# Performance work log

Measured on AMD Instinct MI355X. Metric: run time of the kernel, lower is better.

Reference implementation:

```python
import jax, jax.numpy as jnp
import numpy as np

INNER = 4
AFFECT_W = 0.3
LN_EPS = 1e-5


def _ln(x, w, b):
    m = x.mean(-1, keepdims=True)
    v = ((x - m) ** 2).mean(-1, keepdims=True)
    return (x - m) * jax.lax.rsqrt(v + LN_EPS) * w + b


def _gelu(x):
    return jax.nn.gelu(x, approximate=False)  # torch default erf GELU


def setup_inputs() -> dict:
    key = jax.random.key(0)
    ks = jax.random.split(key, 24)
    B, D = 32768, 128
    s = 0.02
    inp = {
        "x": jax.random.normal(ks[0], (B, D), jnp.float32),
        "y_init": jax.random.normal(ks[1], (B, D), jnp.float32),
        "affect_vec": jax.random.normal(ks[2], (B, 3), jnp.float32),
        # LayerNorms
        "ln_lat_w": jnp.ones((3 * D,), jnp.float32), "ln_lat_b": jnp.zeros((3 * D,), jnp.float32),
        "ln_ans_w": jnp.ones((2 * D,), jnp.float32), "ln_ans_b": jnp.zeros((2 * D,), jnp.float32),
        "ln_z_w": jnp.ones((D,), jnp.float32), "ln_z_b": jnp.zeros((D,), jnp.float32),
        # latent MLP: 3D -> 2D -> D
        "W_lat1": jax.random.normal(ks[3], (3 * D, 2 * D), jnp.float32) * s, "b_lat1": jnp.zeros((2 * D,), jnp.float32),
        "W_lat2": jax.random.normal(ks[4], (2 * D, D), jnp.float32) * s, "b_lat2": jnp.zeros((D,), jnp.float32),
        # answer MLP: 2D -> 2D -> D
        "W_ans1": jax.random.normal(ks[5], (2 * D, 2 * D), jnp.float32) * s, "b_ans1": jnp.zeros((2 * D,), jnp.float32),
        "W_ans2": jax.random.normal(ks[6], (2 * D, D), jnp.float32) * s, "b_ans2": jnp.zeros((D,), jnp.float32),
        # affect proj 3 -> D (tanh), gate 2D -> 1 (sigmoid)
        "W_ap": jax.random.normal(ks[7], (3, D), jnp.float32) * s, "b_ap": jnp.zeros((D,), jnp.float32),
        "W_ag": jax.random.normal(ks[8], (2 * D, 1), jnp.float32) * s, "b_ag": jnp.zeros((1,), jnp.float32),
        # tiny single-head self-attention (q,k,v projections)
        "Wq": jax.random.normal(ks[9], (D, D), jnp.float32) * s, "bq": jnp.zeros((D,), jnp.float32),
        "Wk": jax.random.normal(ks[10], (D, D), jnp.float32) * s, "bk": jnp.zeros((D,), jnp.float32),
        "Wv": jax.random.normal(ks[11], (D, D), jnp.float32) * s, "bv": jnp.zeros((D,), jnp.float32),
        "W_p1": jax.random.normal(ks[12], (D, D // 2), jnp.float32) * s, "b_p1": jnp.zeros((D // 2,), jnp.float32),
        "W_p2": jax.random.normal(ks[13], (D // 2, 3), jnp.float32) * s, "b_p2": jnp.zeros((3,), jnp.float32),
        "K": 5,
    }
    return inp


def reference(x, y_init, affect_vec,
              ln_lat_w, ln_lat_b, ln_ans_w, ln_ans_b, ln_z_w, ln_z_b,
              W_lat1, b_lat1, W_lat2, b_lat2,
              W_ans1, b_ans1, W_ans2, b_ans2,
              W_ap, b_ap, W_ag, b_ag,
              Wq, bq, Wk, bk, Wv, bv,
              W_p1, b_p1, W_p2, b_p2, K):
    D = x.shape[-1]
    scale = 1.0 / jnp.sqrt(jnp.asarray(D, x.dtype))
    y = y_init
    z = jnp.zeros_like(y)
    confs = []
    history = []  # list of [B,1,D]
    for k in range(K):
        for n in range(INNER):
            li = _ln(jnp.concatenate([x, y, z], axis=-1), ln_lat_w, ln_lat_b)
            z_delta = _gelu(li @ W_lat1 + b_lat1) @ W_lat2 + b_lat2
            z = _ln(z + 0.3 * z_delta, ln_z_w, ln_z_b)
        affect_latent = jnp.tanh(affect_vec @ W_ap + b_ap)          # [B,D]
        gate = jax.nn.sigmoid(jnp.concatenate([z, affect_latent], axis=-1) @ W_ag + b_ag)  # [B,1]
        z = z + AFFECT_W * gate * affect_latent
        confs.append(gate.mean())
        history.append(z[:, None, :])
        if len(history) > 1:
            seq = jnp.concatenate(history, axis=1)                   # [B,t,D], t<=K
            q = seq @ Wq + bq
            kk = seq @ Wk + bk
            v = seq @ Wv + bv
            att = jax.nn.softmax(jnp.einsum('btd,bsd->bts', q, kk) * scale, axis=-1)
            attn_out = jnp.einsum('bts,bsd->btd', att, v)
            z = _ln(z + attn_out[:, -1, :], ln_z_w, ln_z_b)
        ai = _ln(jnp.concatenate([y, z], axis=-1), ln_ans_w, ln_ans_b)
        y = y + 0.4 * (_gelu(ai @ W_ans1 + b_ans1) @ W_ans2 + b_ans2)
    pad = jnp.tanh(_gelu(z @ W_p1 + b_p1) @ W_p2 + b_p2)             # [B,3]
    return y, jnp.stack(confs), pad
```

## Files before the change

### kernel.cpp

```cpp
#include <hip/hip_runtime.h>
#include <hip/hip_bf16.h>
#include <math.h>


constexpr int NB = 32768;
constexpr int ND = 128;
constexpr float LNEPS = 1e-5f;

typedef short bf16x8 __attribute__((ext_vector_type(8)));
typedef float f32x4 __attribute__((ext_vector_type(4)));
typedef unsigned uint4v __attribute__((ext_vector_type(4)));
using bf16 = __hip_bfloat16;

static __device__ __forceinline__ float gelu_erf(float x) {
  return 0.5f * x * (1.0f + erff(x * 0.70710678118654752440f));
}
static __device__ __forceinline__ float sigmoidf_(float x) {
  return 1.0f / (1.0f + expf(-x));
}
static __device__ __forceinline__ f32x4 mfma16(bf16x8 a, bf16x8 b, f32x4 c) {
  return __builtin_amdgcn_mfma_f32_16x16x32_bf16(a, b, c, 0, 0, 0);
}
static __device__ __forceinline__ float bfs2f(short u) {
  unsigned v = ((unsigned)(unsigned short)u) << 16;
  return __builtin_bit_cast(float, v);
}
static __device__ __forceinline__ unsigned pk_bf2(float a, float b) {
  unsigned ua = __builtin_bit_cast(unsigned, a);
  unsigned ub = __builtin_bit_cast(unsigned, b);
  ua = (ua + 0x7fffu + ((ua >> 16) & 1u)) >> 16;
  ub = (ub + 0x7fffu + ((ub >> 16) & 1u)) & 0xffff0000u;
  return ub | ua;
}

__global__ void prep_w_frag(const float* __restrict__ src, bf16* __restrict__ dst,
                            int K, int N) {
  int i = blockIdx.x * 256 + threadIdx.x;
  if (i >= K * N) return;
  int k = i / N, n = i - k * N;
  int f = ((n >> 4) * (K >> 5) + (k >> 5)) * 512 + (n & 15) * 32 + (k & 31);
  dst[f] = __float2bfloat16(src[i]);
}

__global__ void prep_w1p(const float* __restrict__ W1, const float* __restrict__ lnw,
                         bf16* __restrict__ WXY, bf16* __restrict__ WZ) {
  int i = blockIdx.x * 256 + threadIdx.x;
  if (i >= 384 * 256) return;
  int j = i >> 8, n = i & 255;
  float v = lnw[j] * W1[i];
  if (j < 256) {
    int f = ((n >> 4) * 8 + (j >> 5)) * 512 + (n & 15) * 32 + (j & 31);
    WXY[f] = __float2bfloat16(v);
  } else {
    int k = j - 256;
    int f = ((n >> 4) * 4 + (k >> 5)) * 512 + (n & 15) * 32 + (k & 31);
    WZ[f] = __float2bfloat16(v);
  }
}

__global__ void prep_uv(const float* __restrict__ W1, const float* __restrict__ lnw,
                        const float* __restrict__ lnb, const float* __restrict__ b1,
                        float* __restrict__ U, float* __restrict__ V0b) {
  int n = threadIdx.x;
  float u = 0.f, v = 0.f;
  for (int j = 0; j < 384; ++j) {
    float w = W1[j * 256 + n];
    u = fmaf(lnw[j], w, u);
    v = fmaf(lnb[j], w, v);
  }
  U[n] = u;
  V0b[n] = v + b1[n];
}

__global__ __launch_bounds__(512) void trm_step(
    const float* __restrict__ x, float* __restrict__ y,
    float* __restrict__ z,
    const bf16* __restrict__ W1XYF, const bf16* __restrict__ W1ZF,
    const float* __restrict__ U, const float* __restrict__ V0b,
    const bf16* __restrict__ W2F, const float* __restrict__ b2,
    const float* __restrict__ lzw, const float* __restrict__ lzb,
    const float* __restrict__ av_g,
    const float* __restrict__ lnw_ans, const float* __restrict__ lnb_ans,
    const bf16* __restrict__ WA1F, const float* __restrict__ ba1,
    const bf16* __restrict__ WA2F, const float* __restrict__ ba2,
    const float* __restrict__ Wap, const float* __restrict__ bap,
    const float* __restrict__ Wag, const float* __restrict__ bag,
    const bf16* __restrict__ WqF, const float* __restrict__ bq,
    const bf16* __restrict__ WkF, const float* __restrict__ bk,
    const bf16* __restrict__ WvF, const float* __restrict__ bv,
    float* __restrict__ gate_sum,
    bf16* __restrict__ kh, bf16* __restrict__ vh, int k)
{
  __shared__ __align__(16) char pool[153600];
  __shared__ float gsum[8];
  float (* const zs)[132] = (float(*)[132])pool;
  float (* const ys)[132] = (float(*)[132])(pool + 33792);
  char* const scr = pool + 67584;
  bf16* const pxy  = (bf16*)scr;
  bf16* const znbL = (bf16*)(scr + 33792);
  bf16* const hx   = (bf16*)(scr + 51200);
  bf16* const znbT = (bf16*)scr;
  bf16* const qvb  = (bf16*)(scr + 17408);
  bf16* const kcb  = (bf16*)(scr + 34816);
  bf16* const vcb  = (bf16*)(scr + 52224);
  bf16* const ai   = (bf16*)scr;
  bf16* const ha   = (bf16*)(scr + 33792);
  float2* const sxy = (float2*)(pool + 152576);
  float2* const mr  = (float2*)(pool + 153088);

  const int t = threadIdx.x;
  const int wave = t >> 6, lane = t & 63;
  const int row8 = t >> 3, sub8 = t & 7;
  const int arow = lane & 15, kseg = (lane >> 4) * 8, crow = (lane >> 4) * 4;
  const size_t row0 = (size_t)blockIdx.x * 64;
  const size_t gr = row0 + row8;

  {
    float s = 0.f, ss = 0.f;
    float4 xv[4], yv[4];
    const float4* xp = (const float4*)&x[gr * ND + sub8 * 16];
    const float4* yp = (const float4*)&y[gr * ND + sub8 * 16];
#pragma unroll
    for (int q = 0; q < 4; ++q) { xv[q] = xp[q]; yv[q] = yp[q]; }
#pragma unroll
    for (int q = 0; q < 4; ++q) {
      s += xv[q].x + xv[q].y + xv[q].z + xv[q].w +
           yv[q].x + yv[q].y + yv[q].z + yv[q].w;
      ss += xv[q].x * xv[q].x + xv[q].y * xv[q].y + xv[q].z * xv[q].z + xv[q].w * xv[q].w +
            yv[q].x * yv[q].x + yv[q].y * yv[q].y + yv[q].z * yv[q].z + yv[q].w * yv[q].w;
    }
#pragma unroll
    for (int q = 0; q < 4; ++q) {
      *(unsigned*)&hx[row8 * 264 + sub8 * 16 + q * 4]       = pk_bf2(xv[q].x, xv[q].y);
      *(unsigned*)&hx[row8 * 264 + sub8 * 16 + q * 4 + 2]   = pk_bf2(xv[q].z, xv[q].w);
      *(unsigned*)&hx[row8 * 264 + 128 + sub8 * 16 + q * 4]     = pk_bf2(yv[q].x, yv[q].y);
      *(unsigned*)&hx[row8 * 264 + 128 + sub8 * 16 + q * 4 + 2] = pk_bf2(yv[q].z, yv[q].w);
      *(float4*)&ys[row8][sub8 * 16 + q * 4] = yv[q];
    }
#pragma unroll
    for (int o = 1; o < 8; o <<= 1) { s += __shfl_xor(s, o); ss += __shfl_xor(ss, o); }

    float zsum = 0.f, zss = 0.f;
    float4 zv[4];
    const float4* zp = (const float4*)&z[gr * ND + sub8 * 16];
#pragma unroll
    for (int q = 0; q < 4; ++q) zv[q] = zp[q];
#pragma unroll
    for (int q = 0; q < 4; ++q) {
      *(float4*)&zs[row8][sub8 * 16 + q * 4] = zv[q];
      *(unsigned*)&znbL[row8 * 136 + sub8 * 16 + q * 4]     = pk_bf2(zv[q].x, zv[q].y);
      *(unsigned*)&znbL[row8 * 136 + sub8 * 16 + q * 4 + 2] = pk_bf2(zv[q].z, zv[q].w);
      zsum += zv[q].x + zv[q].y + zv[q].z + zv[q].w;
      zss += zv[q].x * zv[q].x + zv[q].y * zv[q].y + zv[q].z * zv[q].z + zv[q].w * zv[q].w;
    }
#pragma unroll
    for (int o = 1; o < 8; o <<= 1) { zsum += __shfl_xor(zsum, o); zss += __shfl_xor(zss, o); }
    if (sub8 == 0) {
      sxy[row8] = make_float2(s, ss);
      float mm = (s + zsum) * (1.f / 384.f);
      float var = (ss + zss) * (1.f / 384.f) - mm * mm;
      mr[row8] = make_float2(mm, rsqrtf(var + LNEPS));
    }
  }
  __syncthreads();

  {
    f32x4 acc[4][2];
#pragma unroll
    for (int mi = 0; mi < 4; ++mi)
#pragma unroll
      for (int ni = 0; ni < 2; ++ni) acc[mi][ni] = (f32x4){0.f, 0.f, 0.f, 0.f};
#pragma unroll
    for (int kt = 0; kt < 8; ++kt) {
      bf16x8 a[4];
#pragma unroll
      for (int mi = 0; mi < 4; ++mi)
        a[mi] = *(const bf16x8*)&hx[(mi * 16 + arow) * 264 + kt * 32 + kseg];
#pragma unroll
      for (int ni = 0; ni < 2; ++ni) {
        bf16x8 b = *(const bf16x8*)&W1XYF[(size_t)((wave * 2 + ni) * 8 + kt) * 512 +
                                          arow * 32 + kseg];
        acc[0][ni] = mfma16(a[0], b, acc[0][ni]);
        acc[1][ni] = mfma16(a[1], b, acc[1][ni]);
        acc[2][ni] = mfma16(a[2], b, acc[2][ni]);
        acc[3][ni] = mfma16(a[3], b, acc[3][ni]);
      }
    }
#pragma unroll
    for (int ni = 0; ni < 2; ++ni) {
      int col = (wave * 2 + ni) * 16 + arow;
#pragma unroll
      for (int mi = 0; mi < 4; ++mi)
#pragma unroll
        for (int r = 0; r < 4; ++r)
          pxy[(mi * 16 + crow + r) * 264 + col] = __float2bfloat16(acc[mi][ni][r]);
    }
  }
  __syncthreads();

  float Uv[2], Vv[2];
#pragma unroll
  for (int ni = 0; ni < 2; ++ni) {
    int col = (wave * 2 + ni) * 16 + arow;
    Uv[ni] = U[col];
    Vv[ni] = V0b[col];
  }
  const float b2v = b2[wave * 16 + arow];

  for (int n = 0; n < 4; ++n) {
    {
      f32x4 acc[4][2];
#pragma unroll
      for (int mi = 0; mi < 4; ++mi)
#pragma unroll
        for (int ni = 0; ni < 2; ++ni) acc[mi][ni] = (f32x4){0.f, 0.f, 0.f, 0.f};
#pragma unroll
      for (int kt = 0; kt < 4; ++kt) {
        bf16x8 a[4];
#pragma unroll
        for (int mi = 0; mi < 4; ++mi)
          a[mi] = *(const bf16x8*)&znbL[(mi * 16 + arow) * 136 + kt * 32 + kseg];
#pragma unroll
        for (int ni = 0; ni < 2; ++ni) {
          bf16x8 b = *(const bf16x8*)&W1ZF[(size_t)((wave * 2 + ni) * 4 + kt) * 512 +
                                           arow * 32 + kseg];
          acc[0][ni] = mfma16(a[0], b, acc[0][ni]);
          acc[1][ni] = mfma16(a[1], b, acc[1][ni]);
          acc[2][ni] = mfma16(a[2], b, acc[2][ni]);
          acc[3][ni] = mfma16(a[3], b, acc[3][ni]);
        }
      }
#pragma unroll
      for (int ni = 0; ni < 2; ++ni) {
        int col = (wave * 2 + ni) * 16 + arow;
#pragma unroll
        for (int mi = 0; mi < 4; ++mi)
#pragma unroll
          for (int r = 0; r < 4; ++r) {
            int row = mi * 16 + crow + r;
            float2 mrv = mr[row];
            float pv = __bfloat162float(pxy[row * 264 + col]);
            float hpre = mrv.y * (acc[mi][ni][r] + pv - mrv.x * Uv[ni]) + Vv[ni];
            hx[row * 264 + col] = __float2bfloat16(gelu_erf(hpre));
          }
      }
    }
    __syncthreads();

    {
      f32x4 acc2[4];
#pragma unroll
      for (int mi = 0; mi < 4; ++mi) acc2[mi] = (f32x4){0.f, 0.f, 0.f, 0.f};
#pragma unroll
      for (int kt = 0; kt < 8; ++kt) {
        bf16x8 b = *(const bf16x8*)&W2F[(size_t)(wave * 8 + kt) * 512 + arow * 32 + kseg];
#pragma unroll
        for (int mi = 0; mi < 4; ++mi) {
          bf16x8 a = *(const bf16x8*)&hx[(mi * 16 + arow) * 264 + kt * 32 + kseg];
          acc2[mi] = mfma16(a, b, acc2[mi]);
        }
      }
      int col = wave * 16 + arow;
#pragma unroll
      for (int mi = 0; mi < 4; ++mi)
#pragma unroll
        for (int r = 0; r < 4; ++r)
          zs[mi * 16 + crow + r][col] += 0.3f * (acc2[mi][r] + b2v);
    }
    __syncthreads();

    {
      float4 v[4];
#pragma unroll
      for (int q = 0; q < 4; ++q) v[q] = *(const float4*)&zs[row8][sub8 * 16 + q * 4];
      float s = 0.f, ss = 0.f;
#pragma unroll
      for (int q = 0; q < 4; ++q) {
        s += v[q].x + v[q].y + v[q].z + v[q].w;
        ss += v[q].x * v[q].x + v[q].y * v[q].y + v[q].z * v[q].z + v[q].w * v[q].w;
      }
#pragma unroll
      for (int o = 1; o < 8; o <<= 1) { s += __shfl_xor(s, o); ss += __shfl_xor(ss, o); }
      float m = s * (1.f / 128.f);
      float rstd = rsqrtf(ss * (1.f / 128.f) - m * m + LNEPS);
      float os = 0.f, oss = 0.f;
#pragma unroll
      for (int q = 0; q < 4; ++q) {
        float4 w = *(const float4*)&lzw[sub8 * 16 + q * 4];
        float4 b = *(const float4*)&lzb[sub8 * 16 + q * 4];
        float4 o4;
        o4.x = (v[q].x - m) * rstd * w.x + b.x;
        o4.y = (v[q].y - m) * rstd * w.y + b.y;
        o4.z = (v[q].z - m) * rstd * w.z + b.z;
        o4.w = (v[q].w - m) * rstd * w.w + b.w;
        *(float4*)&zs[row8][sub8 * 16 + q * 4] = o4;
        *(unsigned*)&znbL[row8 * 136 + sub8 * 16 + q * 4]     = pk_bf2(o4.x, o4.y);
        *(unsigned*)&znbL[row8 * 136 + sub8 * 16 + q * 4 + 2] = pk_bf2(o4.z, o4.w);
        os += o4.x + o4.y + o4.z + o4.w;
        oss += o4.x * o4.x + o4.y * o4.y + o4.z * o4.z + o4.w * o4.w;
      }
#pragma unroll
      for (int o = 1; o < 8; o <<= 1) { os += __shfl_xor(os, o); oss += __shfl_xor(oss, o); }
      if (sub8 == 0) {
        float2 sv = sxy[row8];
        float mm = (sv.x + os) * (1.f / 384.f);
        float var = (sv.y + oss) * (1.f / 384.f) - mm * mm;
        mr[row8] = make_float2(mm, rsqrtf(var + LNEPS));
      }
    }
    __syncthreads();
  }

  {
    float zf[16];
#pragma unroll
    for (int q = 0; q < 4; ++q) {
      float4 v = *(const float4*)&zs[row8][sub8 * 16 + q * 4];
      zf[q * 4 + 0] = v.x; zf[q * 4 + 1] = v.y;
      zf[q * 4 + 2] = v.z; zf[q * 4 + 3] = v.w;
    }
    float a0 = av_g[gr * 3 + 0], a1 = av_g[gr * 3 + 1], a2 = av_g[gr * 3 + 2];
    float alf[16];
    float s = 0.f;
#pragma unroll
    for (int e = 0; e < 16; ++e) {
      int c = sub8 * 16 + e;
      alf[e] = tanhf(fmaf(a0, Wap[c], fmaf(a1, Wap[128 + c], fmaf(a2, Wap[256 + c], bap[c]))));
      s += zf[e] * Wag[c] + alf[e] * Wag[128 + c];
    }
#pragma unroll
    for (int o = 1; o < 8; o <<= 1) s += __shfl_xor(s, o);
    float g = sigmoidf_(s + bag[0]);
    float gv = (sub8 == 0) ? g : 0.f;
#pragma unroll
    for (int o = 1; o < 64; o <<= 1) gv += __shfl_xor(gv, o);
    if (lane == 0) gsum[wave] = gv;
#pragma unroll
    for (int e = 0; e < 16; ++e) zf[e] = fmaf(0.3f * g, alf[e], zf[e]);
#pragma unroll
    for (int q = 0; q < 4; ++q) {
      float4 o4;
      o4.x = zf[q * 4 + 0]; o4.y = zf[q * 4 + 1];
      o4.z = zf[q * 4 + 2]; o4.w = zf[q * 4 + 3];
      *(float4*)&zs[row8][sub8 * 16 + q * 4] = o4;
      *(unsigned*)&znbT[row8 * 136 + sub8 * 16 + q * 4]     = pk_bf2(o4.x, o4.y);
      *(unsigned*)&znbT[row8 * 136 + sub8 * 16 + q * 4 + 2] = pk_bf2(o4.z, o4.w);
    }
  }
  __syncthreads();
  if (t == 0) {
    float gs = 0.f;
#pragma unroll
    for (int w = 0; w < 8; ++w) gs += gsum[w];
    atomicAdd(gate_sum + k, gs);
  }

  {
    f32x4 aq[4], ak[4], av2[4];
#pragma unroll
    for (int mi = 0; mi < 4; ++mi) {
      aq[mi] = (f32x4){0.f, 0.f, 0.f, 0.f};
      ak[mi] = (f32x4){0.f, 0.f, 0.f, 0.f};
      av2[mi] = (f32x4){0.f, 0.f, 0.f, 0.f};
    }
#pragma unroll
    for (int kt = 0; kt < 4; ++kt) {
      size_t wr = (size_t)(wave * 4 + kt) * 512 + arow * 32 + kseg;
      bf16x8 bqv = *(const bf16x8*)&WqF[wr];
      bf16x8 bkv = *(const bf16x8*)&WkF[wr];
      bf16x8 bvv = *(const bf16x8*)&WvF[wr];
#pragma unroll
      for (int mi = 0; mi < 4; ++mi) {
        bf16x8 a = *(const bf16x8*)&znbT[(mi * 16 + arow) * 136 + kt * 32 + kseg];
        aq[mi] = mfma16(a, bqv, aq[mi]);
        ak[mi] = mfma16(a, bkv, ak[mi]);
        av2[mi] = mfma16(a, bvv, av2[mi]);
      }
    }
    int col = wave * 16 + arow;
    float bqs = bq[col], bks = bk[col], bvs = bv[col];
#pragma unroll
    for (int mi = 0; mi < 4; ++mi)
#pragma unroll
      for (int r = 0; r < 4; ++r) {
        int row = mi * 16 + crow + r;
        qvb[row * 136 + col] = __float2bfloat16(aq[mi][r] + bqs);
        kcb[row * 136 + col] = __float2bfloat16(ak[mi][r] + bks);
        vcb[row * 136 + col] = __float2bfloat16(av2[mi][r] + bvs);
      }
  }
  __syncthreads();

  if (k < 4) {
    uint4v k0 = *(const uint4v*)&kcb[row8 * 136 + sub8 * 16];
    uint4v k1 = *(const uint4v*)&kcb[row8 * 136 + sub8 * 16 + 8];
    uint4v v0 = *(const uint4v*)&vcb[row8 * 136 + sub8 * 16];
    uint4v v1 = *(const uint4v*)&vcb[row8 * 136 + sub8 * 16 + 8];
    size_t off = ((size_t)k * NB + gr) * ND + sub8 * 16;
    __builtin_nontemporal_store(k0, (uint4v*)&kh[off]);
    __builtin_nontemporal_store(k1, (uint4v*)&kh[off + 8]);
    __builtin_nontemporal_store(v0, (uint4v*)&vh[off]);
    __builtin_nontemporal_store(v1, (uint4v*)&vh[off + 8]);
  }
  {
    float zf[16];
#pragma unroll
    for (int q = 0; q < 4; ++q) {
      float4 v = *(const float4*)&zs[row8][sub8 * 16 + q * 4];
      zf[q * 4 + 0] = v.x; zf[q * 4 + 1] = v.y;
      zf[q * 4 + 2] = v.z; zf[q * 4 + 3] = v.w;
    }
    if (k > 0) {
      bf16x8 qv0 = *(const bf16x8*)&qvb[row8 * 136 + sub8 * 16];
      bf16x8 qv1 = *(const bf16x8*)&qvb[row8 * 136 + sub8 * 16 + 8];
      float p[5];
#pragma unroll
      for (int s = 0; s < 5; ++s) {
        if (s > k) break;
        bf16x8 k0, k1;
        if (s == k) {
          k0 = *(const bf16x8*)&kcb[row8 * 136 + sub8 * 16];
          k1 = *(const bf16x8*)&kcb[row8 * 136 + sub8 * 16 + 8];
        } else {
          size_t off = ((size_t)s * NB + gr) * ND + sub8 * 16;
          k0 = __builtin_bit_cast(bf16x8, __builtin_nontemporal_load((const uint4v*)&kh[off]));
          k1 = __builtin_bit_cast(bf16x8, __builtin_nontemporal_load((const uint4v*)&kh[off + 8]));
        }
        float d = 0.f;
#pragma unroll
        for (int e = 0; e < 8; ++e)
          d += bfs2f(qv0[e]) * bfs2f(k0[e]) + bfs2f(qv1[e]) * bfs2f(k1[e]);
#pragma unroll
        for (int o = 1; o < 8; o <<= 1) d += __shfl_xor(d, o);
        p[s] = d * 0.088388347648318447f;
      }
      float mx = p[0];
#pragma unroll
      for (int s = 1; s < 5; ++s) if (s <= k) mx = fmaxf(mx, p[s]);
      float sum = 0.f;
#pragma unroll
      for (int s = 0; s < 5; ++s) if (s <= k) { p[s] = expf(p[s] - mx); sum += p[s]; }
      float inv = 1.f / sum;
      float ao[16];
#pragma unroll
      for (int e = 0; e < 16; ++e) ao[e] = 0.f;
#pragma unroll
      for (int s = 0; s < 5; ++s) {
        if (s > k) break;
        bf16x8 v0, v1;
        if (s == k) {
          v0 = *(const bf16x8*)&vcb[row8 * 136 + sub8 * 16];
          v1 = *(const bf16x8*)&vcb[row8 * 136 + sub8 * 16 + 8];
        } else {
          size_t off = ((size_t)s * NB + gr) * ND + sub8 * 16;
          v0 = __builtin_bit_cast(bf16x8, __builtin_nontemporal_load((const uint4v*)&vh[off]));
          v1 = __builtin_bit_cast(bf16x8, __builtin_nontemporal_load((const uint4v*)&vh[off + 8]));
        }
        float w = p[s] * inv;
#pragma unroll
        for (int e = 0; e < 8; ++e) {
          ao[e]     = fmaf(w, bfs2f(v0[e]), ao[e]);
          ao[8 + e] = fmaf(w, bfs2f(v1[e]), ao[8 + e]);
        }
      }
#pragma unroll
      for (int e = 0; e < 16; ++e) zf[e] += ao[e];
      float s2 = 0.f, ss = 0.f;
#pragma unroll
      for (int e = 0; e < 16; ++e) { s2 += zf[e]; ss += zf[e] * zf[e]; }
#pragma unroll
      for (int o = 1; o < 8; o <<= 1) { s2 += __shfl_xor(s2, o); ss += __shfl_xor(ss, o); }
      float m = s2 * (1.f / 128.f);
      float rstd = rsqrtf(ss * (1.f / 128.f) - m * m + LNEPS);
#pragma unroll
      for (int e = 0; e < 16; ++e) {
        int c = sub8 * 16 + e;
        zf[e] = (zf[e] - m) * rstd * lzw[c] + lzb[c];
      }
#pragma unroll
      for (int q = 0; q < 4; ++q) {
        float4 o4;
        o4.x = zf[q * 4 + 0]; o4.y = zf[q * 4 + 1];
        o4.z = zf[q * 4 + 2]; o4.w = zf[q * 4 + 3];
        *(float4*)&zs[row8][sub8 * 16 + q * 4] = o4;
      }
    }
#pragma unroll
    for (int q = 0; q < 4; ++q) {
      float4 o4;
      o4.x = zf[q * 4 + 0]; o4.y = zf[q * 4 + 1];
      o4.z = zf[q * 4 + 2]; o4.w = zf[q * 4 + 3];
      *(float4*)&z[gr * ND + sub8 * 16 + q * 4] = o4;
    }
  }
  __syncthreads();

  {
    float yf[16], zf[16];
#pragma unroll
    for (int q = 0; q < 4; ++q) {
      float4 v = *(const float4*)&ys[row8][sub8 * 16 + q * 4];
      yf[q * 4 + 0] = v.x; yf[q * 4 + 1] = v.y;
      yf[q * 4 + 2] = v.z; yf[q * 4 + 3] = v.w;
      float4 w = *(const float4*)&zs[row8][sub8 * 16 + q * 4];
      zf[q * 4 + 0] = w.x; zf[q * 4 + 1] = w.y;
      zf[q * 4 + 2] = w.z; zf[q * 4 + 3] = w.w;
    }
    float s = 0.f, ss = 0.f;
#pragma unroll
    for (int e = 0; e < 16; ++e) {
      s += yf[e] + zf[e];
      ss += yf[e] * yf[e] + zf[e] * zf[e];
    }
#pragma unroll
    for (int o = 1; o < 8; o <<= 1) { s += __shfl_xor(s, o); ss += __shfl_xor(ss, o); }
    float m = s * (1.f / 256.f);
    float rstd = rsqrtf(ss * (1.f / 256.f) - m * m + LNEPS);
#pragma unroll
    for (int h = 0; h < 2; ++h) {
      const float* vp = (h == 0) ? yf : zf;
#pragma unroll
      for (int q = 0; q < 4; ++q) {
        int c0 = h * 128 + sub8 * 16 + q * 4;
        float a0 = (vp[q * 4 + 0] - m) * rstd * lnw_ans[c0 + 0] + lnb_ans[c0 + 0];
        float a1 = (vp[q * 4 + 1] - m) * rstd * lnw_ans[c0 + 1] + lnb_ans[c0 + 1];
        float a2 = (vp[q * 4 + 2] - m) * rstd * lnw_ans[c0 + 2] + lnb_ans[c0 + 2];
        float a3 = (vp[q * 4 + 3] - m) * rstd * lnw_ans[c0 + 3] + lnb_ans[c0 + 3];
        *(unsigned*)&ai[row8 * 264 + c0]     = pk_bf2(a0, a1);
        *(unsigned*)&ai[row8 * 264 + c0 + 2] = pk_bf2(a2, a3);
      }
    }
  }
  __syncthreads();

  {
    f32x4 acc[4][2];
#pragma unroll
    for (int mi = 0; mi < 4; ++mi)
#pragma unroll
      for (int ni = 0; ni < 2; ++ni) acc[mi][ni] = (f32x4){0.f, 0.f, 0.f, 0.f};
#pragma unroll
    for (int kt = 0; kt < 8; ++kt) {
      bf16x8 a[4];
#pragma unroll
      for (int mi = 0; mi < 4; ++mi)
        a[mi] = *(const bf16x8*)&ai[(mi * 16 + arow) * 264 + kt * 32 + kseg];
#pragma unroll
      for (int ni = 0; ni < 2; ++ni) {
        bf16x8 b = *(const bf16x8*)&WA1F[(size_t)((wave * 2 + ni) * 8 + kt) * 512 +
                                         arow * 32 + kseg];
        acc[0][ni] = mfma16(a[0], b, acc[0][ni]);
        acc[1][ni] = mfma16(a[1], b, acc[1][ni]);
        acc[2][ni] = mfma16(a[2], b, acc[2][ni]);
        acc[3][ni] = mfma16(a[3], b, acc[3][ni]);
      }
    }
#pragma unroll
    for (int ni = 0; ni < 2; ++ni) {
      int col = (wave * 2 + ni) * 16 + arow;
      float bb = ba1[col];
#pragma unroll
      for (int mi = 0; mi < 4; ++mi)
#pragma unroll
        for (int r = 0; r < 4; ++r)
          ha[(mi * 16 + crow + r) * 264 + col] =
              __float2bfloat16(gelu_erf(acc[mi][ni][r] + bb));
    }
  }
  __syncthreads();

  {
    f32x4 acc[4];
#pragma unroll
    for (int mi = 0; mi < 4; ++mi) acc[mi] = (f32x4){0.f, 0.f, 0.f, 0.f};
#pragma unroll
    for (int kt = 0; kt < 8; ++kt) {
      bf16x8 b = *(const bf16x8*)&WA2F[(size_t)(wave * 8 + kt) * 512 + arow * 32 + kseg];
#pragma unroll
      for (int mi = 0; mi < 4; ++mi) {
        bf16x8 a = *(const bf16x8*)&ha[(mi * 16 + arow) * 264 + kt * 32 + kseg];
        acc[mi] = mfma16(a, b, acc[mi]);
      }
    }
    int col = wave * 16 + arow;
    float bb = ba2[col];
#pragma unroll
    for (int mi = 0; mi < 4; ++mi)
#pragma unroll
      for (int r = 0; r < 4; ++r)
        ys[mi * 16 + crow + r][col] += 0.4f * (acc[mi][r] + bb);
  }
  __syncthreads();

#pragma unroll
  for (int q = 0; q < 4; ++q)
    *(float4*)&y[gr * ND + sub8 * 16 + q * 4] =
        *(const float4*)&ys[row8][sub8 * 16 + q * 4];
}

__global__ __launch_bounds__(256) void pad_head(
    const float* __restrict__ z,
    const float* __restrict__ W1, const float* __restrict__ b1,
    const float* __restrict__ W2, const float* __restrict__ b2,
    float* __restrict__ out)
{
  __shared__ __align__(16) float zsm[32][132];
  __shared__ __align__(16) float h[32][68];
  const int t = threadIdx.x;
  const int row0 = blockIdx.x * 32;
  {
    const int c = t & 127, rg = t >> 7;
#pragma unroll
    for (int r16 = 0; r16 < 16; ++r16) {
      int r = rg * 16 + r16;
      zsm[r][c] = z[(size_t)(row0 + r) * ND + c];
    }
  }
  __syncthreads();
  {
    const int c = t & 63, rg8 = t >> 6;
    float acc[8];
#pragma unroll
    for (int r = 0; r < 8; ++r) acc[r] = 0.f;
    for (int j0 = 0; j0 < ND; j0 += 4) {
      float w0 = W1[(j0 + 0) * 64 + c], w1 = W1[(j0 + 1) * 64 + c];
      float w2 = W1[(j0 + 2) * 64 + c], w3 = W1[(j0 + 3) * 64 + c];
#pragma unroll
      for (int r = 0; r < 8; ++r) {
        float4 a = *reinterpret_cast<const float4*>(&zsm[rg8 * 8 + r][j0]);
        acc[r] = fmaf(a.x, w0, fmaf(a.y, w1, fmaf(a.z, w2, fmaf(a.w, w3, acc[r]))));
      }
    }
    float bb = b1[c];
#pragma unroll
    for (int r = 0; r < 8; ++r) h[rg8 * 8 + r][c] = gelu_erf(acc[r] + bb);
  }
  __syncthreads();
  {
    const int row = t >> 3, sub = t & 7;
    if (sub < 3) {
      float p = 0.f;
      for (int j = 0; j < 64; ++j) p += h[row][j] * W2[j * 3 + sub];
      out[(size_t)(row0 + row) * 3 + sub] = tanhf(p + b2[sub]);
    }
  }
}

__global__ void finalize_confs(const float* __restrict__ gs, float* __restrict__ confs) {
  int i = threadIdx.x;
  if (i < 5) confs[i] = gs[i] * (1.0f / 32768.0f);
}

extern "C" void kernel_launch(void* const* d_in, const int* in_sizes, int n_in,
                              void* d_out, int out_size, void* d_ws, size_t ws_size,
                              hipStream_t stream) {
  const float* x       = (const float*)d_in[0];
  const float* y_init  = (const float*)d_in[1];
  const float* av      = (const float*)d_in[2];
  const float* ln_lat_w = (const float*)d_in[3];
  const float* ln_lat_b = (const float*)d_in[4];
  const float* ln_ans_w = (const float*)d_in[5];
  const float* ln_ans_b = (const float*)d_in[6];
  const float* ln_z_w   = (const float*)d_in[7];
  const float* ln_z_b   = (const float*)d_in[8];
  const float* W_lat1 = (const float*)d_in[9];  const float* b_lat1 = (const float*)d_in[10];
  const float* W_lat2 = (const float*)d_in[11]; const float* b_lat2 = (const float*)d_in[12];
  const float* W_ans1 = (const float*)d_in[13]; const float* b_ans1 = (const float*)d_in[14];
  const float* W_ans2 = (const float*)d_in[15]; const float* b_ans2 = (const float*)d_in[16];
  const float* W_ap = (const float*)d_in[17];   const float* b_ap = (const float*)d_in[18];
  const float* W_ag = (const float*)d_in[19];   const float* b_ag = (const float*)d_in[20];
  const float* Wq = (const float*)d_in[21];     const float* bq = (const float*)d_in[22];
  const float* Wk = (const float*)d_in[23];     const float* bk = (const float*)d_in[24];
  const float* Wv = (const float*)d_in[25];     const float* bv = (const float*)d_in[26];
  const float* W_p1 = (const float*)d_in[27];   const float* b_p1 = (const float*)d_in[28];
  const float* W_p2 = (const float*)d_in[29];   const float* b_p2 = (const float*)d_in[30];

  float* y     = (float*)d_out;
  float* confs = (float*)d_out + (size_t)NB * ND;
  float* pad   = confs + 5;

  char* p = (char*)d_ws;
  float* gate_sum = (float*)p;
  float* z   = (float*)(p + 256);
  bf16* kh   = (bf16*)(p + 256 + (size_t)NB * ND * 4);
  bf16* vh   = kh + (size_t)4 * NB * ND;
  bf16* W2F  = vh + (size_t)4 * NB * ND;
  bf16* WA1F = W2F + 256 * 128;
  bf16* WA2F = WA1F + 256 * 256;
  bf16* WqF  = WA2F + 256 * 128;
  bf16* WkF  = WqF + 128 * 128;
  bf16* WvF  = WkF + 128 * 128;
  bf16* W1XYF = WvF + 128 * 128;
  bf16* W1ZF  = W1XYF + 256 * 256;
  float* U    = (float*)(W1ZF + 128 * 256);
  float* V0b  = U + 256;

  hipMemcpyAsync(y, y_init, (size_t)NB * ND * sizeof(float),
                 hipMemcpyDeviceToDevice, stream);
  hipMemsetAsync(gate_sum, 0, 32, stream);
  hipMemsetAsync(z, 0, (size_t)NB * ND * sizeof(float), stream);

  prep_w1p<<<(384 * 256 + 255) / 256, 256, 0, stream>>>(W_lat1, ln_lat_w, W1XYF, W1ZF);
  prep_uv<<<1, 256, 0, stream>>>(W_lat1, ln_lat_w, ln_lat_b, b_lat1, U, V0b);
  prep_w_frag<<<(256 * 128 + 255) / 256, 256, 0, stream>>>(W_lat2, W2F, 256, 128);
  prep_w_frag<<<(256 * 256 + 255) / 256, 256, 0, stream>>>(W_ans1, WA1F, 256, 256);
  prep_w_frag<<<(256 * 128 + 255) / 256, 256, 0, stream>>>(W_ans2, WA2F, 256, 128);
  prep_w_frag<<<(128 * 128 + 255) / 256, 256, 0, stream>>>(Wq, WqF, 128, 128);
  prep_w_frag<<<(128 * 128 + 255) / 256, 256, 0, stream>>>(Wk, WkF, 128, 128);
  prep_w_frag<<<(128 * 128 + 255) / 256, 256, 0, stream>>>(Wv, WvF, 128, 128);

  for (int k = 0; k < 5; ++k) {
    trm_step<<<NB / 64, 512, 0, stream>>>(
        x, y, z, W1XYF, W1ZF, U, V0b, W2F, b_lat2, ln_z_w, ln_z_b,
        av, ln_ans_w, ln_ans_b,
        WA1F, b_ans1, WA2F, b_ans2,
        W_ap, b_ap, W_ag, b_ag,
        WqF, bq, WkF, bk, WvF, bv,
        gate_sum, kh, vh, k);
  }
  pad_head<<<NB / 32, 256, 0, stream>>>(z, W_p1, b_p1, W_p2, b_p2, pad);
  finalize_confs<<<1, 64, 0, stream>>>(gate_sum, confs);
}
```

Baseline: 800.7 us.

## Shrink trm_step blocks to 32 rows and 4 waves to fit two blocks per CU

Each block of the fused step kernel now handles 32 rows with 256 threads instead of 64 rows with 512. The shared-memory pool is halved and the buffers are re-laid out so that two blocks can be resident per CU. Each wave now computes a 2x4 or 2x2 MFMA tile across more output columns instead of a 4x2 tile, so the work is split across waves differently. The aim is better latency hiding and overlap across blocks, at the cost of each block reading the weight fragments twice as often relative to the rows it processes.

```diff
diff --git a/kernel.cpp b/kernel.cpp
--- a/kernel.cpp
+++ b/kernel.cpp
@@ -72,7 +72,7 @@
   V0b[n] = v + b1[n];
 }
 
-__global__ __launch_bounds__(512) void trm_step(
+__global__ __launch_bounds__(256) void trm_step(
     const float* __restrict__ x, float* __restrict__ y,
     float* __restrict__ z,
     const bf16* __restrict__ W1XYF, const bf16* __restrict__ W1ZF,
@@ -91,28 +91,27 @@
     float* __restrict__ gate_sum,
     bf16* __restrict__ kh, bf16* __restrict__ vh, int k)
 {
-  __shared__ __align__(16) char pool[153600];
-  __shared__ float gsum[8];
+  __shared__ __align__(16) char pool[76800];
+  __shared__ float gsum[4];
   float (* const zs)[132] = (float(*)[132])pool;
-  float (* const ys)[132] = (float(*)[132])(pool + 33792);
-  char* const scr = pool + 67584;
-  bf16* const pxy  = (bf16*)scr;
-  bf16* const znbL = (bf16*)(scr + 33792);
-  bf16* const hx   = (bf16*)(scr + 51200);
-  bf16* const znbT = (bf16*)scr;
-  bf16* const qvb  = (bf16*)(scr + 17408);
-  bf16* const kcb  = (bf16*)(scr + 34816);
-  bf16* const vcb  = (bf16*)(scr + 52224);
-  bf16* const ai   = (bf16*)scr;
-  bf16* const ha   = (bf16*)(scr + 33792);
-  float2* const sxy = (float2*)(pool + 152576);
-  float2* const mr  = (float2*)(pool + 153088);
+  float (* const ys)[132] = (float(*)[132])(pool + 16896);
+  char* const scr = pool + 33792;
+  bf16* const znbL = (bf16*)scr;
+  bf16* const hx   = (bf16*)(scr + 8704);
+  bf16* const pxy  = (bf16*)(scr + 25600);
+  bf16* const qvb  = (bf16*)(scr + 8704);
+  bf16* const kcb  = (bf16*)(scr + 17408);
+  bf16* const vcb  = (bf16*)(scr + 26112);
+  bf16* const ai   = (bf16*)(scr + 8704);
+  bf16* const ha   = (bf16*)(scr + 25600);
+  float2* const sxy = (float2*)(pool + 76288);
+  float2* const mr  = (float2*)(pool + 76544);
 
   const int t = threadIdx.x;
   const int wave = t >> 6, lane = t & 63;
   const int row8 = t >> 3, sub8 = t & 7;
   const int arow = lane & 15, kseg = (lane >> 4) * 8, crow = (lane >> 4) * 4;
-  const size_t row0 = (size_t)blockIdx.x * 64;
+  const size_t row0 = (size_t)blockIdx.x * 32;
   const size_t gr = row0 + row8;
 
   {
@@ -165,32 +164,28 @@
   __syncthreads();
 
   {
-    f32x4 acc[4][2];
-#pragma unroll
-    for (int mi = 0; mi < 4; ++mi)
-#pragma unroll
-      for (int ni = 0; ni < 2; ++ni) acc[mi][ni] = (f32x4){0.f, 0.f, 0.f, 0.f};
+    f32x4 acc[2][4];
+#pragma unroll
+    for (int mi = 0; mi < 2; ++mi)
+#pragma unroll
+      for (int ni = 0; ni < 4; ++ni) acc[mi][ni] = (f32x4){0.f, 0.f, 0.f, 0.f};
 #pragma unroll
     for (int kt = 0; kt < 8; ++kt) {
-      bf16x8 a[4];
-#pragma unroll
-      for (int mi = 0; mi < 4; ++mi)
-        a[mi] = *(const bf16x8*)&hx[(mi * 16 + arow) * 264 + kt * 32 + kseg];
-#pragma unroll
-      for (int ni = 0; ni < 2; ++ni) {
-        bf16x8 b = *(const bf16x8*)&W1XYF[(size_t)((wave * 2 + ni) * 8 + kt) * 512 +
+      bf16x8 a0 = *(const bf16x8*)&hx[arow * 264 + kt * 32 + kseg];
+      bf16x8 a1 = *(const bf16x8*)&hx[(16 + arow) * 264 + kt * 32 + kseg];
+#pragma unroll
+      for (int ni = 0; ni < 4; ++ni) {
+        bf16x8 b = *(const bf16x8*)&W1XYF[(size_t)((wave * 4 + ni) * 8 + kt) * 512 +
                                           arow * 32 + kseg];
-        acc[0][ni] = mfma16(a[0], b, acc[0][ni]);
-        acc[1][ni] = mfma16(a[1], b, acc[1][ni]);
-        acc[2][ni] = mfma16(a[2], b, acc[2][ni]);
-        acc[3][ni] = mfma16(a[3], b, acc[3][ni]);
-      }
-    }
-#pragma unroll
-    for (int ni = 0; ni < 2; ++ni) {
-      int col = (wave * 2 + ni) * 16 + arow;
-#pragma unroll
-      for (int mi = 0; mi < 4; ++mi)
+        acc[0][ni] = mfma16(a0, b, acc[0][ni]);
+        acc[1][ni] = mfma16(a1, b, acc[1][ni]);
+      }
+    }
+#pragma unroll
+    for (int ni = 0; ni < 4; ++ni) {
+      int col = (wave * 4 + ni) * 16 + arow;
+#pragma unroll
+      for (int mi = 0; mi < 2; ++mi)
 #pragma unroll
         for (int r = 0; r < 4; ++r)
           pxy[(mi * 16 + crow + r) * 264 + col] = __float2bfloat16(acc[mi][ni][r]);
@@ -198,43 +193,40 @@
   }
   __syncthreads();
 
-  float Uv[2], Vv[2];
-#pragma unroll
-  for (int ni = 0; ni < 2; ++ni) {
-    int col = (wave * 2 + ni) * 16 + arow;
+  float Uv[4], Vv[4], b2v[2];
+#pragma unroll
+  for (int ni = 0; ni < 4; ++ni) {
+    int col = (wave * 4 + ni) * 16 + arow;
     Uv[ni] = U[col];
     Vv[ni] = V0b[col];
   }
-  const float b2v = b2[wave * 16 + arow];
+#pragma unroll
+  for (int ni = 0; ni < 2; ++ni) b2v[ni] = b2[(wave * 2 + ni) * 16 + arow];
 
   for (int n = 0; n < 4; ++n) {
     {
-      f32x4 acc[4][2];
-#pragma unroll
-      for (int mi = 0; mi < 4; ++mi)
-#pragma unroll
-        for (int ni = 0; ni < 2; ++ni) acc[mi][ni] = (f32x4){0.f, 0.f, 0.f, 0.f};
+      f32x4 acc[2][4];
+#pragma unroll
+      for (int mi = 0; mi < 2; ++mi)
+#pragma unroll
+        for (int ni = 0; ni < 4; ++ni) acc[mi][ni] = (f32x4){0.f, 0.f, 0.f, 0.f};
 #pragma unroll
       for (int kt = 0; kt < 4; ++kt) {
-        bf16x8 a[4];
-#pragma unroll
-        for (int mi = 0; mi < 4; ++mi)
-          a[mi] = *(const bf16x8*)&znbL[(mi * 16 + arow) * 136 + kt * 32 + kseg];
-#pragma unroll
-        for (int ni = 0; ni < 2; ++ni) {
-          bf16x8 b = *(const bf16x8*)&W1ZF[(size_t)((wave * 2 + ni) * 4 + kt) * 512 +
+        bf16x8 a0 = *(const bf16x8*)&znbL[arow * 136 + kt * 32 + kseg];
+        bf16x8 a1 = *(const bf16x8*)&znbL[(16 + arow) * 136 + kt * 32 + kseg];
+#pragma unroll
+        for (int ni = 0; ni < 4; ++ni) {
+          bf16x8 b = *(const bf16x8*)&W1ZF[(size_t)((wave * 4 + ni) * 4 + kt) * 512 +
                                            arow * 32 + kseg];
-          acc[0][ni] = mfma16(a[0], b, acc[0][ni]);
-          acc[1][ni] = mfma16(a[1], b, acc[1][ni]);
-          acc[2][ni] = mfma16(a[2], b, acc[2][ni]);
-          acc[3][ni] = mfma16(a[3], b, acc[3][ni]);
+          acc[0][ni] = mfma16(a0, b, acc[0][ni]);
+          acc[1][ni] = mfma16(a1, b, acc[1][ni]);
         }
       }
 #pragma unroll
-      for (int ni = 0; ni < 2; ++ni) {
-        int col = (wave * 2 + ni) * 16 + arow;
-#pragma unroll
-        for (int mi = 0; mi < 4; ++mi)
+      for (int ni = 0; ni < 4; ++ni) {
+        int col = (wave * 4 + ni) * 16 + arow;
+#pragma unroll
+        for (int mi = 0; mi < 2; ++mi)
 #pragma unroll
           for (int r = 0; r < 4; ++r) {
             int row = mi * 16 + crow + r;
@@ -248,24 +240,32 @@
     __syncthreads();
 
     {
-      f32x4 acc2[4];
-#pragma unroll
-      for (int mi = 0; mi < 4; ++mi) acc2[mi] = (f32x4){0.f, 0.f, 0.f, 0.f};
+      f32x4 acc2[2][2];
+#pragma unroll
+      for (int mi = 0; mi < 2; ++mi)
+#pragma unroll
+        for (int ni = 0; ni < 2; ++ni) acc2[mi][ni] = (f32x4){0.f, 0.f, 0.f, 0.f};
 #pragma unroll
       for (int kt = 0; kt < 8; ++kt) {
-        bf16x8 b = *(const bf16x8*)&W2F[(size_t)(wave * 8 + kt) * 512 + arow * 32 + kseg];
-#pragma unroll
-        for (int mi = 0; mi < 4; ++mi) {
-          bf16x8 a = *(const bf16x8*)&hx[(mi * 16 + arow) * 264 + kt * 32 + kseg];
-          acc2[mi] = mfma16(a, b, acc2[mi]);
+        bf16x8 a0 = *(const bf16x8*)&hx[arow * 264 + kt * 32 + kseg];
+        bf16x8 a1 = *(const bf16x8*)&hx[(16 + arow) * 264 + kt * 32 + kseg];
+#pragma unroll
+        for (int ni = 0; ni < 2; ++ni) {
+          bf16x8 b = *(const bf16x8*)&W2F[(size_t)((wave * 2 + ni) * 8 + kt) * 512 +
+                                          arow * 32 + kseg];
+          acc2[0][ni] = mfma16(a0, b, acc2[0][ni]);
+          acc2[1][ni] = mfma16(a1, b, acc2[1][ni]);
         }
       }
-      int col = wave * 16 + arow;
-#pragma unroll
-      for (int mi = 0; mi < 4; ++mi)
-#pragma unroll
-        for (int r = 0; r < 4; ++r)
-          zs[mi * 16 + crow + r][col] += 0.3f * (acc2[mi][r] + b2v);
+#pragma unroll
+      for (int ni = 0; ni < 2; ++ni) {
+        int col = (wave * 2 + ni) * 16 + arow;
+#pragma unroll
+        for (int mi = 0; mi < 2; ++mi)
+#pragma unroll
+          for (int r = 0; r < 4; ++r)
+            zs[mi * 16 + crow + r][col] += 0.3f * (acc2[mi][ni][r] + b2v[ni]);
+      }
     }
     __syncthreads();
 
@@ -343,51 +343,55 @@
       o4.x = zf[q * 4 + 0]; o4.y = zf[q * 4 + 1];
       o4.z = zf[q * 4 + 2]; o4.w = zf[q * 4 + 3];
       *(float4*)&zs[row8][sub8 * 16 + q * 4] = o4;
-      *(unsigned*)&znbT[row8 * 136 + sub8 * 16 + q * 4]     = pk_bf2(o4.x, o4.y);
-      *(unsigned*)&znbT[row8 * 136 + sub8 * 16 + q * 4 + 2] = pk_bf2(o4.z, o4.w);
+      *(unsigned*)&znbL[row8 * 136 + sub8 * 16 + q * 4]     = pk_bf2(o4.x, o4.y);
+      *(unsigned*)&znbL[row8 * 136 + sub8 * 16 + q * 4 + 2] = pk_bf2(o4.z, o4.w);
     }
   }
   __syncthreads();
   if (t == 0) {
-    float gs = 0.f;
-#pragma unroll
-    for (int w = 0; w < 8; ++w) gs += gsum[w];
+    float gs = gsum[0] + gsum[1] + gsum[2] + gsum[3];
     atomicAdd(gate_sum + k, gs);
   }
 
   {
-    f32x4 aq[4], ak[4], av2[4];
-#pragma unroll
-    for (int mi = 0; mi < 4; ++mi) {
-      aq[mi] = (f32x4){0.f, 0.f, 0.f, 0.f};
-      ak[mi] = (f32x4){0.f, 0.f, 0.f, 0.f};
-      av2[mi] = (f32x4){0.f, 0.f, 0.f, 0.f};
-    }
+    f32x4 aq[2][2], ak[2][2], av2[2][2];
+#pragma unroll
+    for (int mi = 0; mi < 2; ++mi)
+#pragma unroll
+      for (int ni = 0; ni < 2; ++ni) {
+        aq[mi][ni] = (f32x4){0.f, 0.f, 0.f, 0.f};
+        ak[mi][ni] = (f32x4){0.f, 0.f, 0.f, 0.f};
+        av2[mi][ni] = (f32x4){0.f, 0.f, 0.f, 0.f};
+      }
 #pragma unroll
     for (int kt = 0; kt < 4; ++kt) {
-      size_t wr = (size_t)(wave * 4 + kt) * 512 + arow * 32 + kseg;
-      bf16x8 bqv = *(const bf16x8*)&WqF[wr];
-      bf16x8 bkv = *(const bf16x8*)&WkF[wr];
-      bf16x8 bvv = *(const bf16x8*)&WvF[wr];
-#pragma unroll
-      for (int mi = 0; mi < 4; ++mi) {
-        bf16x8 a = *(const bf16x8*)&znbT[(mi * 16 + arow) * 136 + kt * 32 + kseg];
-        aq[mi] = mfma16(a, bqv, aq[mi]);
-        ak[mi] = mfma16(a, bkv, ak[mi]);
-        av2[mi] = mfma16(a, bvv, av2[mi]);
-      }
-    }
-    int col = wave * 16 + arow;
-    float bqs = bq[col], bks = bk[col], bvs = bv[col];
-#pragma unroll
-    for (int mi = 0; mi < 4; ++mi)
-#pragma unroll
-      for (int r = 0; r < 4; ++r) {
-        int row = mi * 16 + crow + r;
-        qvb[row * 136 + col] = __float2bfloat16(aq[mi][r] + bqs);
-        kcb[row * 136 + col] = __float2bfloat16(ak[mi][r] + bks);
-        vcb[row * 136 + col] = __float2bfloat16(av2[mi][r] + bvs);
-      }
+      bf16x8 a0 = *(const bf16x8*)&znbL[arow * 136 + kt * 32 + kseg];
+      bf16x8 a1 = *(const bf16x8*)&znbL[(16 + arow) * 136 + kt * 32 + kseg];
+#pragma unroll
+      for (int ni = 0; ni < 2; ++ni) {
+        size_t wr = (size_t)((wave * 2 + ni) * 4 + kt) * 512 + arow * 32 + kseg;
+        bf16x8 bqv = *(const bf16x8*)&WqF[wr];
+        bf16x8 bkv = *(const bf16x8*)&WkF[wr];
+        bf16x8 bvv = *(const bf16x8*)&WvF[wr];
+        aq[0][ni] = mfma16(a0, bqv, aq[0][ni]);   aq[1][ni] = mfma16(a1, bqv, aq[1][ni]);
+        ak[0][ni] = mfma16(a0, bkv, ak[0][ni]);   ak[1][ni] = mfma16(a1, bkv, ak[1][ni]);
+        av2[0][ni] = mfma16(a0, bvv, av2[0][ni]); av2[1][ni] = mfma16(a1, bvv, av2[1][ni]);
+      }
+    }
+#pragma unroll
+    for (int ni = 0; ni < 2; ++ni) {
+      int col = (wave * 2 + ni) * 16 + arow;
+      float bqs = bq[col], bks = bk[col], bvs = bv[col];
+#pragma unroll
+      for (int mi = 0; mi < 2; ++mi)
+#pragma unroll
+        for (int r = 0; r < 4; ++r) {
+          int row = mi * 16 + crow + r;
+          qvb[row * 136 + col] = __float2bfloat16(aq[mi][ni][r] + bqs);
+          kcb[row * 136 + col] = __float2bfloat16(ak[mi][ni][r] + bks);
+          vcb[row * 136 + col] = __float2bfloat16(av2[mi][ni][r] + bvs);
+        }
+    }
   }
   __syncthreads();
 
@@ -534,33 +538,29 @@
   __syncthreads();
 
   {
-    f32x4 acc[4][2];
-#pragma unroll
-    for (int mi = 0; mi < 4; ++mi)
-#pragma unroll
-      for (int ni = 0; ni < 2; ++ni) acc[mi][ni] = (f32x4){0.f, 0.f, 0.f, 0.f};
+    f32x4 acc[2][4];
+#pragma unroll
+    for (int mi = 0; mi < 2; ++mi)
+#pragma unroll
+      for (int ni = 0; ni < 4; ++ni) acc[mi][ni] = (f32x4){0.f, 0.f, 0.f, 0.f};
 #pragma unroll
     for (int kt = 0; kt < 8; ++kt) {
-      bf16x8 a[4];
-#pragma unroll
-      for (int mi = 0; mi < 4; ++mi)
-        a[mi] = *(const bf16x8*)&ai[(mi * 16 + arow) * 264 + kt * 32 + kseg];
-#pragma unroll
-      for (int ni = 0; ni < 2; ++ni) {
-        bf16x8 b = *(const bf16x8*)&WA1F[(size_t)((wave * 2 + ni) * 8 + kt) * 512 +
+      bf16x8 a0 = *(const bf16x8*)&ai[arow * 264 + kt * 32 + kseg];
+      bf16x8 a1 = *(const bf16x8*)&ai[(16 + arow) * 264 + kt * 32 + kseg];
+#pragma unroll
+      for (int ni = 0; ni < 4; ++ni) {
+        bf16x8 b = *(const bf16x8*)&WA1F[(size_t)((wave * 4 + ni) * 8 + kt) * 512 +
                                          arow * 32 + kseg];
-        acc[0][ni] = mfma16(a[0], b, acc[0][ni]);
-        acc[1][ni] = mfma16(a[1], b, acc[1][ni]);
-        acc[2][ni] = mfma16(a[2], b, acc[2][ni]);
-        acc[3][ni] = mfma16(a[3], b, acc[3][ni]);
-      }
-    }
-#pragma unroll
-    for (int ni = 0; ni < 2; ++ni) {
-      int col = (wave * 2 + ni) * 16 + arow;
+        acc[0][ni] = mfma16(a0, b, acc[0][ni]);
+        acc[1][ni] = mfma16(a1, b, acc[1][ni]);
+      }
+    }
+#pragma unroll
+    for (int ni = 0; ni < 4; ++ni) {
+      int col = (wave * 4 + ni) * 16 + arow;
       float bb = ba1[col];
 #pragma unroll
-      for (int mi = 0; mi < 4; ++mi)
+      for (int mi = 0; mi < 2; ++mi)
 #pragma unroll
         for (int r = 0; r < 4; ++r)
           ha[(mi * 16 + crow + r) * 264 + col] =
@@ -570,25 +570,33 @@
   __syncthreads();
 
   {
-    f32x4 acc[4];
-#pragma unroll
-    for (int mi = 0; mi < 4; ++mi) acc[mi] = (f32x4){0.f, 0.f, 0.f, 0.f};
+    f32x4 acc[2][2];
+#pragma unroll
+    for (int mi = 0; mi < 2; ++mi)
+#pragma unroll
+      for (int ni = 0; ni < 2; ++ni) acc[mi][ni] = (f32x4){0.f, 0.f, 0.f, 0.f};
 #pragma unroll
     for (int kt = 0; kt < 8; ++kt) {
-      bf16x8 b = *(const bf16x8*)&WA2F[(size_t)(wave * 8 + kt) * 512 + arow * 32 + kseg];
-#pragma unroll
-      for (int mi = 0; mi < 4; ++mi) {
-        bf16x8 a = *(const bf16x8*)&ha[(mi * 16 + arow) * 264 + kt * 32 + kseg];
-        acc[mi] = mfma16(a, b, acc[mi]);
-      }
-    }
-    int col = wave * 16 + arow;
-    float bb = ba2[col];
-#pragma unroll
-    for (int mi = 0; mi < 4; ++mi)
-#pragma unroll
-      for (int r = 0; r < 4; ++r)
-        ys[mi * 16 + crow + r][col] += 0.4f * (acc[mi][r] + bb);
+      bf16x8 a0 = *(const bf16x8*)&ha[arow * 264 + kt * 32 + kseg];
+      bf16x8 a1 = *(const bf16x8*)&ha[(16 + arow) * 264 + kt * 32 + kseg];
+#pragma unroll
+      for (int ni = 0; ni < 2; ++ni) {
+        bf16x8 b = *(const bf16x8*)&WA2F[(size_t)((wave * 2 + ni) * 8 + kt) * 512 +
+                                         arow * 32 + kseg];
+        acc[0][ni] = mfma16(a0, b, acc[0][ni]);
+        acc[1][ni] = mfma16(a1, b, acc[1][ni]);
+      }
+    }
+#pragma unroll
+    for (int ni = 0; ni < 2; ++ni) {
+      int col = (wave * 2 + ni) * 16 + arow;
+      float bb = ba2[col];
+#pragma unroll
+      for (int mi = 0; mi < 2; ++mi)
+#pragma unroll
+        for (int r = 0; r < 4; ++r)
+          ys[mi * 16 + crow + r][col] += 0.4f * (acc[mi][ni][r] + bb);
+    }
   }
   __syncthreads();
 
@@ -710,7 +718,7 @@
   prep_w_frag<<<(128 * 128 + 255) / 256, 256, 0, stream>>>(Wv, WvF, 128, 128);
 
   for (int k = 0; k < 5; ++k) {
-    trm_step<<<NB / 64, 512, 0, stream>>>(
+    trm_step<<<NB / 32, 256, 0, stream>>>(
         x, y, z, W1XYF, W1ZF, U, V0b, W2F, b_lat2, ln_z_w, ln_z_b,
         av, ln_ans_w, ln_ans_b,
         WA1F, b_ans1, WA2F, b_ans2,
```

After: 1.094 ms. +36.6%, slower.

## Fuse PAD head into last step and skip z memset and reload

Applied to the files above, without the earlier changes.

The PAD regression head now runs inside the final trm_step launch, reading z from shared memory instead of a separate kernel re-reading z from global memory. The z zero memset is removed: step 0 synthesizes zeros instead of loading, and the last step no longer writes z back. Attention accumulation now goes straight into zf, dropping a temporary array. This removes one launch plus about 32 MB of z traffic, at the cost of extra code and registers in the hot kernel.

```diff
diff --git a/kernel.cpp b/kernel.cpp
--- a/kernel.cpp
+++ b/kernel.cpp
@@ -88,6 +88,9 @@
     const bf16* __restrict__ WqF, const float* __restrict__ bq,
     const bf16* __restrict__ WkF, const float* __restrict__ bk,
     const bf16* __restrict__ WvF, const float* __restrict__ bv,
+    const float* __restrict__ Wp1, const float* __restrict__ bp1,
+    const float* __restrict__ Wp2, const float* __restrict__ bp2,
+    float* __restrict__ pad_out,
     float* __restrict__ gate_sum,
     bf16* __restrict__ kh, bf16* __restrict__ vh, int k)
 {
@@ -105,6 +108,7 @@
   bf16* const vcb  = (bf16*)(scr + 52224);
   bf16* const ai   = (bf16*)scr;
   bf16* const ha   = (bf16*)(scr + 33792);
+  float* const h1  = (float*)scr;
   float2* const sxy = (float2*)(pool + 152576);
   float2* const mr  = (float2*)(pool + 153088);
 
@@ -142,9 +146,14 @@
 
     float zsum = 0.f, zss = 0.f;
     float4 zv[4];
-    const float4* zp = (const float4*)&z[gr * ND + sub8 * 16];
-#pragma unroll
-    for (int q = 0; q < 4; ++q) zv[q] = zp[q];
+    if (k > 0) {
+      const float4* zp = (const float4*)&z[gr * ND + sub8 * 16];
+#pragma unroll
+      for (int q = 0; q < 4; ++q) zv[q] = zp[q];
+    } else {
+#pragma unroll
+      for (int q = 0; q < 4; ++q) zv[q] = (float4){0.f, 0.f, 0.f, 0.f};
+    }
 #pragma unroll
     for (int q = 0; q < 4; ++q) {
       *(float4*)&zs[row8][sub8 * 16 + q * 4] = zv[q];
@@ -441,9 +450,6 @@
 #pragma unroll
       for (int s = 0; s < 5; ++s) if (s <= k) { p[s] = expf(p[s] - mx); sum += p[s]; }
       float inv = 1.f / sum;
-      float ao[16];
-#pragma unroll
-      for (int e = 0; e < 16; ++e) ao[e] = 0.f;
 #pragma unroll
       for (int s = 0; s < 5; ++s) {
         if (s > k) break;
@@ -459,12 +465,10 @@
         float w = p[s] * inv;
 #pragma unroll
         for (int e = 0; e < 8; ++e) {
-          ao[e]     = fmaf(w, bfs2f(v0[e]), ao[e]);
-          ao[8 + e] = fmaf(w, bfs2f(v1[e]), ao[8 + e]);
+          zf[e]     = fmaf(w, bfs2f(v0[e]), zf[e]);
+          zf[8 + e] = fmaf(w, bfs2f(v1[e]), zf[8 + e]);
         }
       }
-#pragma unroll
-      for (int e = 0; e < 16; ++e) zf[e] += ao[e];
       float s2 = 0.f, ss = 0.f;
 #pragma unroll
       for (int e = 0; e < 16; ++e) { s2 += zf[e]; ss += zf[e] * zf[e]; }
@@ -485,12 +489,14 @@
         *(float4*)&zs[row8][sub8 * 16 + q * 4] = o4;
       }
     }
-#pragma unroll
-    for (int q = 0; q < 4; ++q) {
-      float4 o4;
-      o4.x = zf[q * 4 + 0]; o4.y = zf[q * 4 + 1];
-      o4.z = zf[q * 4 + 2]; o4.w = zf[q * 4 + 3];
-      *(float4*)&z[gr * ND + sub8 * 16 + q * 4] = o4;
+    if (k < 4) {
+#pragma unroll
+      for (int q = 0; q < 4; ++q) {
+        float4 o4;
+        o4.x = zf[q * 4 + 0]; o4.y = zf[q * 4 + 1];
+        o4.z = zf[q * 4 + 2]; o4.w = zf[q * 4 + 3];
+        *(float4*)&z[gr * ND + sub8 * 16 + q * 4] = o4;
+      }
     }
   }
   __syncthreads();
@@ -596,52 +602,35 @@
   for (int q = 0; q < 4; ++q)
     *(float4*)&y[gr * ND + sub8 * 16 + q * 4] =
         *(const float4*)&ys[row8][sub8 * 16 + q * 4];
-}
-
-__global__ __launch_bounds__(256) void pad_head(
-    const float* __restrict__ z,
-    const float* __restrict__ W1, const float* __restrict__ b1,
-    const float* __restrict__ W2, const float* __restrict__ b2,
-    float* __restrict__ out)
-{
-  __shared__ __align__(16) float zsm[32][132];
-  __shared__ __align__(16) float h[32][68];
-  const int t = threadIdx.x;
-  const int row0 = blockIdx.x * 32;
-  {
-    const int c = t & 127, rg = t >> 7;
-#pragma unroll
-    for (int r16 = 0; r16 < 16; ++r16) {
-      int r = rg * 16 + r16;
-      zsm[r][c] = z[(size_t)(row0 + r) * ND + c];
-    }
-  }
-  __syncthreads();
-  {
-    const int c = t & 63, rg8 = t >> 6;
-    float acc[8];
-#pragma unroll
-    for (int r = 0; r < 8; ++r) acc[r] = 0.f;
-    for (int j0 = 0; j0 < ND; j0 += 4) {
-      float w0 = W1[(j0 + 0) * 64 + c], w1 = W1[(j0 + 1) * 64 + c];
-      float w2 = W1[(j0 + 2) * 64 + c], w3 = W1[(j0 + 3) * 64 + c];
-#pragma unroll
-      for (int r = 0; r < 8; ++r) {
-        float4 a = *reinterpret_cast<const float4*>(&zsm[rg8 * 8 + r][j0]);
-        acc[r] = fmaf(a.x, w0, fmaf(a.y, w1, fmaf(a.z, w2, fmaf(a.w, w3, acc[r]))));
-      }
-    }
-    float bb = b1[c];
-#pragma unroll
-    for (int r = 0; r < 8; ++r) h[rg8 * 8 + r][c] = gelu_erf(acc[r] + bb);
-  }
-  __syncthreads();
-  {
-    const int row = t >> 3, sub = t & 7;
-    if (sub < 3) {
-      float p = 0.f;
-      for (int j = 0; j < 64; ++j) p += h[row][j] * W2[j * 3 + sub];
-      out[(size_t)(row0 + row) * 3 + sub] = tanhf(p + b2[sub]);
+
+  if (k == 4) {
+    __syncthreads();
+    {
+      const int cc = t & 63, rg8 = t >> 6;
+      float acc[8];
+#pragma unroll
+      for (int r = 0; r < 8; ++r) acc[r] = 0.f;
+      for (int j0 = 0; j0 < ND; j0 += 4) {
+        float w0 = Wp1[(j0 + 0) * 64 + cc], w1 = Wp1[(j0 + 1) * 64 + cc];
+        float w2 = Wp1[(j0 + 2) * 64 + cc], w3 = Wp1[(j0 + 3) * 64 + cc];
+#pragma unroll
+        for (int r = 0; r < 8; ++r) {
+          float4 a = *reinterpret_cast<const float4*>(&zs[rg8 * 8 + r][j0]);
+          acc[r] = fmaf(a.x, w0, fmaf(a.y, w1, fmaf(a.z, w2, fmaf(a.w, w3, acc[r]))));
+        }
+      }
+      float bb = bp1[cc];
+#pragma unroll
+      for (int r = 0; r < 8; ++r) h1[(rg8 * 8 + r) * 68 + cc] = gelu_erf(acc[r] + bb);
+    }
+    __syncthreads();
+    {
+      const int row = t >> 3, sub = t & 7;
+      if (sub < 3) {
+        float p = 0.f;
+        for (int j = 0; j < 64; ++j) p += h1[row * 68 + j] * Wp2[j * 3 + sub];
+        pad_out[(row0 + row) * 3 + sub] = tanhf(p + bp2[sub]);
+      }
     }
   }
 }
@@ -698,7 +687,6 @@
   hipMemcpyAsync(y, y_init, (size_t)NB * ND * sizeof(float),
                  hipMemcpyDeviceToDevice, stream);
   hipMemsetAsync(gate_sum, 0, 32, stream);
-  hipMemsetAsync(z, 0, (size_t)NB * ND * sizeof(float), stream);
 
   prep_w1p<<<(384 * 256 + 255) / 256, 256, 0, stream>>>(W_lat1, ln_lat_w, W1XYF, W1ZF);
   prep_uv<<<1, 256, 0, stream>>>(W_lat1, ln_lat_w, ln_lat_b, b_lat1, U, V0b);
@@ -716,8 +704,8 @@
         WA1F, b_ans1, WA2F, b_ans2,
         W_ap, b_ap, W_ag, b_ag,
         WqF, bq, WkF, bk, WvF, bv,
+        W_p1, b_p1, W_p2, b_p2, pad,
         gate_sum, kh, vh, k);
   }
-  pad_head<<<NB / 32, 256, 0, stream>>>(z, W_p1, b_p1, W_p2, b_p2, pad);
   finalize_confs<<<1, 64, 0, stream>>>(gate_sum, confs);
 }
```

Result: no change. 786.3 us (-1.8%).
